# Kernel optimization log

Measured on AMD Instinct MI355X. Metric: run time of the kernel, lower is better.

## Reference

```python
import jax, jax.numpy as jnp
import numpy as np

N, NODE_DIM, EDGE_DIM, HID, NREL = 1024, 128, 32, 128, 16


def _sage(h, adj, W, b):
    # agg = mean over (weighted) neighbors: (adj @ h) / (deg + 1e-6)
    agg = (adj @ h) / (jnp.sum(adj, axis=1, keepdims=True) + 1e-6)
    return jax.nn.relu(jnp.concatenate([h, agg], axis=1) @ W.T + b)


def setup_inputs() -> dict:
    key = jax.random.key(0)
    ks = jax.random.split(key, 12)
    s1 = 1.0 / np.sqrt(2 * NODE_DIM)
    s2 = 1.0 / np.sqrt(2 * HID)
    s3 = 1.0 / np.sqrt(2 * HID + EDGE_DIM)
    s4 = 1.0 / np.sqrt(HID)
    return {
        "node_feat": jax.random.normal(ks[0], (N, NODE_DIM), jnp.float32),
        "edge_feat": jax.random.normal(ks[1], (N, N, EDGE_DIM), jnp.float32),
        "adj": jax.random.uniform(ks[2], (N, N), jnp.float32),
        "W_g1": jax.random.normal(ks[3], (HID, 2 * NODE_DIM), jnp.float32) * s1,
        "b_g1": jax.random.normal(ks[4], (HID,), jnp.float32) * s1,
        "W_g2": jax.random.normal(ks[5], (HID, 2 * HID), jnp.float32) * s2,
        "b_g2": jax.random.normal(ks[6], (HID,), jnp.float32) * s2,
        "W_c1": jax.random.normal(ks[7], (HID, 2 * HID + EDGE_DIM), jnp.float32) * s3,
        "b_c1": jax.random.normal(ks[8], (HID,), jnp.float32) * s3,
        "W_c2": jax.random.normal(ks[9], (NREL, HID), jnp.float32) * s4,
        "b_c2": jax.random.normal(ks[10], (NREL,), jnp.float32) * s4,
    }


def reference(node_feat, edge_feat, adj, W_g1, b_g1, W_g2, b_g2, W_c1, b_c1, W_c2, b_c2):
    h = _sage(node_feat, adj, W_g1, b_g1)          # [N, HID]
    h = _sage(h, adj, W_g2, b_g2)                  # [N, HID]
    H = h.shape[1]
    # Split first classifier layer over [h_i ; h_j ; e_ij] to avoid a huge concat.
    Wa, Wb, We = W_c1[:, :H], W_c1[:, H:2 * H], W_c1[:, 2 * H:]
    pre = ((h @ Wa.T)[:, None, :]
           + (h @ Wb.T)[None, :, :]
           + jnp.einsum('ije,he->ijh', edge_feat, We)
           + b_c1)                                  # [N, N, HID]
    logits = jax.nn.relu(pre) @ W_c2.T + b_c2       # [N, N, NREL]
    # diagonal (i == j) stays zero, matching the skipped loop iterations
    n = logits.shape[0]
    mask = 1.0 - jnp.eye(n, dtype=logits.dtype)
    return logits * mask[:, :, None]
```

## Files before the change

kernel.cpp:

```cpp
#include <hip/hip_runtime.h>
#include <hip/hip_bf16.h>
#include <stdint.h>

constexpr int NN = 1024;
constexpr int DD = 128;
constexpr int EDIM = 32;
constexpr int NR = 16;

using short4v = __attribute__((ext_vector_type(4))) short;
using short8v = __attribute__((ext_vector_type(8))) short;
using f32x4   = __attribute__((ext_vector_type(4))) float;

__device__ __forceinline__ short f2bf(float x) {
  __hip_bfloat16 h = __float2bfloat16(x);
  return __builtin_bit_cast(short, h);
}

__device__ __forceinline__ void gl_lds16(const void* g, void* l) {
  __builtin_amdgcn_global_load_lds(
      (const __attribute__((address_space(1))) unsigned int*)(uintptr_t)g,
      (__attribute__((address_space(3))) unsigned int*)(uint32_t)(uintptr_t)l,
      16, 0, 0);
}

__global__ __launch_bounds__(256) void k_rowsum(const float* __restrict__ adj,
                                                float* __restrict__ rsinv) {
  int i = blockIdx.x, t = threadIdx.x;
  const float4* row = (const float4*)(adj + (size_t)i * NN);
  float4 v = row[t];
  float s = v.x + v.y + v.z + v.w;
  #pragma unroll
  for (int off = 32; off > 0; off >>= 1) s += __shfl_down(s, off, 64);
  __shared__ float red[4];
  if ((t & 63) == 0) red[t >> 6] = s;
  __syncthreads();
  if (t == 0) rsinv[i] = 1.0f / (red[0] + red[1] + red[2] + red[3] + 1e-6f);
}

__global__ __launch_bounds__(256) void k_adjgemm(const float* __restrict__ adj,
                                                 const float* __restrict__ X,
                                                 float* __restrict__ part) {
  __shared__ float sadj[16][128];
  int t = threadIdx.x;
  int ic = blockIdx.x & 63, kc = blockIdx.x >> 6;
  int i0 = ic * 16, k0 = kc * 128;
  {
    int il = t >> 4;
    int kl = (t & 15) * 8;
    const float4* src = (const float4*)(adj + (size_t)(i0 + il) * NN + k0 + kl);
    *(float4*)&sadj[il][kl]     = src[0];
    *(float4*)&sadj[il][kl + 4] = src[1];
  }
  __syncthreads();
  int h = t & 127, ii = t >> 7;
  float acc[8] = {0,0,0,0,0,0,0,0};
  for (int k = 0; k < 128; k += 4) {
    float x0 = X[(size_t)(k0 + k) * DD + h];
    float x1 = X[(size_t)(k0 + k + 1) * DD + h];
    float x2 = X[(size_t)(k0 + k + 2) * DD + h];
    float x3 = X[(size_t)(k0 + k + 3) * DD + h];
    #pragma unroll
    for (int m = 0; m < 8; ++m) {
      int il = ii + m * 2;
      float4 a = *(const float4*)&sadj[il][k];
      acc[m] += a.x * x0 + a.y * x1 + a.z * x2 + a.w * x3;
    }
  }
  #pragma unroll
  for (int m = 0; m < 8; ++m)
    part[((size_t)kc * NN + (i0 + ii + m * 2)) * DD + h] = acc[m];
}

__global__ __launch_bounds__(256) void k_dense2f(const float* __restrict__ X,
                                                 const float* __restrict__ part,
                                                 const float* __restrict__ rsinv,
                                                 const float* __restrict__ W,
                                                 const float* __restrict__ b,
                                                 float* __restrict__ out) {
  __shared__ float sagg[2][128];
  int t = threadIdx.x;
  int ig = t >> 7, h = t & 127;
  int i = blockIdx.x * 2 + ig;
  {
    float s = 0.f;
    #pragma unroll
    for (int kc = 0; kc < 8; ++kc) s += part[(size_t)kc * NN * DD + (size_t)i * DD + h];
    sagg[ig][h] = s * rsinv[i];
  }
  __syncthreads();
  const float4* xr = (const float4*)(X + (size_t)i * DD);
  const float4* ar = (const float4*)(&sagg[ig][0]);
  const float4* w1 = (const float4*)(W + (size_t)h * 256);
  const float4* w2 = (const float4*)(W + (size_t)h * 256 + DD);
  float acc = b[h];
  #pragma unroll 8
  for (int k = 0; k < 32; ++k) {
    float4 x = xr[k], w = w1[k];
    acc += x.x * w.x + x.y * w.y + x.z * w.z + x.w * w.w;
  }
  #pragma unroll 8
  for (int k = 0; k < 32; ++k) {
    float4 y = ar[k], w = w2[k];
    acc += y.x * w.x + y.y * w.y + y.z * w.z + y.w * w.w;
  }
  out[(size_t)i * DD + h] = fmaxf(acc, 0.f);
}

__global__ __launch_bounds__(256) void k_ab(const float* __restrict__ h2,
                                            const float* __restrict__ Wc1,
                                            const float* __restrict__ bc1,
                                            float* __restrict__ Aib,
                                            float* __restrict__ Bmat) {
  int t = threadIdx.x;
  int i = blockIdx.x * 2 + (t >> 7), h = t & 127;
  const float4* xr = (const float4*)(h2 + (size_t)i * DD);
  const float4* wa = (const float4*)(Wc1 + (size_t)h * 288);
  const float4* wb = (const float4*)(Wc1 + (size_t)h * 288 + 128);
  float aa = bc1[h], bb = 0.f;
  #pragma unroll 8
  for (int k = 0; k < 32; ++k) {
    float4 x = xr[k];
    float4 a = wa[k], b2 = wb[k];
    aa += x.x * a.x + x.y * a.y + x.z * a.z + x.w * a.w;
    bb += x.x * b2.x + x.y * b2.y + x.z * b2.z + x.w * b2.w;
  }
  Aib[(size_t)i * DD + h] = aa;
  Bmat[(size_t)i * DD + h] = bb;
}


#define EDGE_BODY(T, OFF, VMN) do {                                           \
    float4 e0_, e1_;                                                          \
    asm volatile("s_waitcnt vmcnt(" #VMN ")\n\t"                              \
                 "ds_read_b128 %0, %2 offset:" #OFF "\n\t"                    \
                 "ds_read_b128 %1, %3 offset:" #OFF "\n\t"                    \
                 "s_waitcnt lgkmcnt(0)"                                       \
                 : "=&v"(e0_), "=&v"(e1_)                                     \
                 : "v"(ea0), "v"(ea1)                                         \
                 : "memory");                                                 \
    __builtin_amdgcn_sched_barrier(0);                                        \
    { int tpf_ = (T) + 3 > 15 ? 15 : (T) + 3;                                 \
      const char* src_ = ebl + (size_t)tpf_ * 131072;                         \
      gl_lds16(src_, esw + (OFF));                                            \
      gl_lds16(src_ + 1024, esw + (OFF) + 1024); }                            \
    __builtin_amdgcn_sched_barrier(0);                                        \
    short8v ef_;                                                              \
    ef_[0]=f2bf(e0_.x); ef_[1]=f2bf(e0_.y); ef_[2]=f2bf(e0_.z); ef_[3]=f2bf(e0_.w); \
    ef_[4]=f2bf(e1_.x); ef_[5]=f2bf(e1_.y); ef_[6]=f2bf(e1_.z); ef_[7]=f2bf(e1_.w); \
    int i_ = i0 + (T);                                                        \
    const float* ap_ = aibs + (T) * 128 + 4 * g;                              \
    _Pragma("unroll")                                                         \
    for (int n = 0; n < 8; ++n) {                                             \
      float4 av_ = *(const float4*)(ap_ + 16 * n);                            \
      f32x4 ci_;                                                              \
      ci_[0] = av_.x + bjv[n].x; ci_[1] = av_.y + bjv[n].y;                   \
      ci_[2] = av_.z + bjv[n].z; ci_[3] = av_.w + bjv[n].w;                   \
      f32x4 acc_ = __builtin_amdgcn_mfma_f32_16x16x32_bf16(weF[n], ef_, ci_, 0, 0, 0); \
      short4v pk_;                                                            \
      pk_[0] = f2bf(fmaxf(acc_[0], 0.f)); pk_[1] = f2bf(fmaxf(acc_[1], 0.f)); \
      pk_[2] = f2bf(fmaxf(acc_[2], 0.f)); pk_[3] = f2bf(fmaxf(acc_[3], 0.f)); \
      *(short4v*)(psm + (((n >> 1) << 10) + ((n & 1) << 9) + wroff)) = pk_;   \
    }                                                                         \
    f32x4 acc2_;                                                              \
    acc2_[0] = bc2v.x; acc2_[1] = bc2v.y; acc2_[2] = bc2v.z; acc2_[3] = bc2v.w; \
    _Pragma("unroll")                                                         \
    for (int kk = 0; kk < 4; ++kk) {                                          \
      short8v pb_ = *(short8v*)(psm + ((kk << 10) + rdP));                    \
      acc2_ = __builtin_amdgcn_mfma_f32_16x16x32_bf16(wcF[kk], pb_, acc2_, 0, 0, 0); \
    }                                                                         \
    bool diag_ = (j == i_);                                                   \
    float4 o_;                                                                \
    o_.x = diag_ ? 0.f : acc2_[0];                                            \
    o_.y = diag_ ? 0.f : acc2_[1];                                            \
    o_.z = diag_ ? 0.f : acc2_[2];                                            \
    o_.w = diag_ ? 0.f : acc2_[3];                                            \
    *(float4*)(out + ((size_t)i_ * NN + j) * NR + 4 * g) = o_;                \
  } while (0)

__global__ __launch_bounds__(256, 3) void k_edge(const float* __restrict__ edge,
                                                 const float* __restrict__ Wc1,
                                                 const float* __restrict__ Wc2,
                                                 const float* __restrict__ bc2,
                                                 const float* __restrict__ Aib,
                                                 const float* __restrict__ Bmat,
                                                 float* __restrict__ out) {
  __shared__ __align__(16) char esm[4][3][2048];
  __shared__ __align__(16) char psm_all[4][4096];
  __shared__ __align__(16) float aibs[16 * 128];
  int tid = threadIdx.x;
  int w = tid >> 6, lane = tid & 63;
  int c = lane & 15, g = lane >> 4;
  int ig = blockIdx.x >> 4, jg = blockIdx.x & 15;
  int i0 = ig * 16;
  int j0w = jg * 64 + w * 16;
  int j = j0w + c;

  {
    int ii = tid >> 4, h8 = (tid & 15) * 8;
    const float4* s = (const float4*)(Aib + (size_t)(i0 + ii) * DD + h8);
    *(float4*)(aibs + ii * 128 + h8)     = s[0];
    *(float4*)(aibs + ii * 128 + h8 + 4) = s[1];
  }
  __syncthreads();

  short8v weF[8];
  #pragma unroll
  for (int n = 0; n < 8; ++n) {
    const float* p = Wc1 + (size_t)(16 * n + c) * 288 + 256 + 8 * g;
    float4 f0 = *(const float4*)p;
    float4 f1 = *(const float4*)(p + 4);
    short8v s;
    s[0]=f2bf(f0.x); s[1]=f2bf(f0.y); s[2]=f2bf(f0.z); s[3]=f2bf(f0.w);
    s[4]=f2bf(f1.x); s[5]=f2bf(f1.y); s[6]=f2bf(f1.z); s[7]=f2bf(f1.w);
    weF[n] = s;
  }
  short8v wcF[4];
  #pragma unroll
  for (int kk = 0; kk < 4; ++kk) {
    const float* p = Wc2 + (size_t)c * DD + 32 * kk + 8 * g;
    float4 f0 = *(const float4*)p;
    float4 f1 = *(const float4*)(p + 4);
    short8v s;
    s[0]=f2bf(f0.x); s[1]=f2bf(f0.y); s[2]=f2bf(f0.z); s[3]=f2bf(f0.w);
    s[4]=f2bf(f1.x); s[5]=f2bf(f1.y); s[6]=f2bf(f1.z); s[7]=f2bf(f1.w);
    wcF[kk] = s;
  }
  float4 bc2v = *(const float4*)(bc2 + 4 * g);
  float4 bjv[8];
  #pragma unroll
  for (int n = 0; n < 8; ++n)
    bjv[n] = *(const float4*)(Bmat + (size_t)j * DD + 16 * n + 4 * g);

  char* esw = &esm[w][0][0];
  char* psm = &psm_all[w][0];
  const char* ebl = (const char*)edge + ((size_t)i0 * NN + j0w) * (EDIM * 4)
                    + ((lane * 16) ^ (((lane >> 3) & 7) << 4));
  int rd0 = c * 128 + ((g * 32)      ^ ((c & 7) << 4));
  int rd1 = c * 128 + ((g * 32 + 16) ^ ((c & 7) << 4));
  int ldsb = (int)(uint32_t)(uintptr_t)esw;
  int ea0 = ldsb + rd0;
  int ea1 = ldsb + rd1;
  int wroff = (c << 4) + ((g & 1) << 3) + ((g >> 1) << 8);
  int rdP   = (g << 8) + (c << 4);

  gl_lds16(ebl,                  esw);
  gl_lds16(ebl + 1024,           esw + 1024);
  gl_lds16(ebl + 131072,         esw + 2048);
  gl_lds16(ebl + 131072 + 1024,  esw + 3072);
  gl_lds16(ebl + 262144,         esw + 4096);
  gl_lds16(ebl + 262144 + 1024,  esw + 5120);

  EDGE_BODY(0, 0, 4);
  EDGE_BODY(1, 2048, 5);
  EDGE_BODY(2, 4096, 6);
  #pragma unroll 1
  for (int t = 3; t < 15; t += 3) {
    EDGE_BODY(t,     0, 6);
    EDGE_BODY(t + 1, 2048, 6);
    EDGE_BODY(t + 2, 4096, 6);
  }
  EDGE_BODY(15, 0, 6);
}

extern "C" void kernel_launch(void* const* d_in, const int* in_sizes, int n_in,
                              void* d_out, int out_size, void* d_ws, size_t ws_size,
                              hipStream_t stream) {
  const float* node_feat = (const float*)d_in[0];
  const float* edge_feat = (const float*)d_in[1];
  const float* adj  = (const float*)d_in[2];
  const float* W_g1 = (const float*)d_in[3];
  const float* b_g1 = (const float*)d_in[4];
  const float* W_g2 = (const float*)d_in[5];
  const float* b_g2 = (const float*)d_in[6];
  const float* W_c1 = (const float*)d_in[7];
  const float* b_c1 = (const float*)d_in[8];
  const float* W_c2 = (const float*)d_in[9];
  const float* b_c2 = (const float*)d_in[10];
  float* out = (float*)d_out;

  float* ws    = (float*)d_ws;
  float* rsinv = ws;
  float* part  = ws + 1024;
  float* h1    = part + 8 * NN * DD;
  float* h2    = h1 + NN * DD;
  float* Aib   = h2 + NN * DD;
  float* Bmat  = Aib + NN * DD;

  k_rowsum<<<NN, 256, 0, stream>>>(adj, rsinv);
  k_adjgemm<<<512, 256, 0, stream>>>(adj, node_feat, part);
  k_dense2f<<<512, 256, 0, stream>>>(node_feat, part, rsinv, W_g1, b_g1, h1);
  k_adjgemm<<<512, 256, 0, stream>>>(adj, h1, part);
  k_dense2f<<<512, 256, 0, stream>>>(h1, part, rsinv, W_g2, b_g2, h2);
  k_ab<<<512, 256, 0, stream>>>(h2, W_c1, b_c1, Aib, Bmat);
  k_edge<<<1024, 256, 0, stream>>>(edge_feat, W_c1, W_c2, b_c2, Aib, Bmat, out);
}
```

Baseline: 139.9 us.

## Deepen edge prefetch pipeline, software-pipeline second MFMA, fuse small prologue kernels

```diff
diff --git a/kernel.cpp b/kernel.cpp
--- a/kernel.cpp
+++ b/kernel.cpp
@@ -21,20 +21,6 @@
       (const __attribute__((address_space(1))) unsigned int*)(uintptr_t)g,
       (__attribute__((address_space(3))) unsigned int*)(uint32_t)(uintptr_t)l,
       16, 0, 0);
-}
-
-__global__ __launch_bounds__(256) void k_rowsum(const float* __restrict__ adj,
-                                                float* __restrict__ rsinv) {
-  int i = blockIdx.x, t = threadIdx.x;
-  const float4* row = (const float4*)(adj + (size_t)i * NN);
-  float4 v = row[t];
-  float s = v.x + v.y + v.z + v.w;
-  #pragma unroll
-  for (int off = 32; off > 0; off >>= 1) s += __shfl_down(s, off, 64);
-  __shared__ float red[4];
-  if ((t & 63) == 0) red[t >> 6] = s;
-  __syncthreads();
-  if (t == 0) rsinv[i] = 1.0f / (red[0] + red[1] + red[2] + red[3] + 1e-6f);
 }
 
 __global__ __launch_bounds__(256) void k_adjgemm(const float* __restrict__ adj,
@@ -71,21 +57,34 @@
     part[((size_t)kc * NN + (i0 + ii + m * 2)) * DD + h] = acc[m];
 }
 
-__global__ __launch_bounds__(256) void k_dense2f(const float* __restrict__ X,
-                                                 const float* __restrict__ part,
-                                                 const float* __restrict__ rsinv,
-                                                 const float* __restrict__ W,
-                                                 const float* __restrict__ b,
-                                                 float* __restrict__ out) {
+__global__ __launch_bounds__(256) void k_dense1(const float* __restrict__ X,
+                                                const float* __restrict__ part,
+                                                const float* __restrict__ adj,
+                                                const float* __restrict__ W,
+                                                const float* __restrict__ b,
+                                                float* __restrict__ out,
+                                                float* __restrict__ rsinv) {
   __shared__ float sagg[2][128];
+  __shared__ float red[4];
   int t = threadIdx.x;
   int ig = t >> 7, h = t & 127;
   int i = blockIdx.x * 2 + ig;
   {
-    float s = 0.f;
+    const float4* ar = (const float4*)(adj + (size_t)i * NN);
+    float4 v0 = ar[h * 2], v1 = ar[h * 2 + 1];
+    float s = v0.x + v0.y + v0.z + v0.w + v1.x + v1.y + v1.z + v1.w;
     #pragma unroll
-    for (int kc = 0; kc < 8; ++kc) s += part[(size_t)kc * NN * DD + (size_t)i * DD + h];
-    sagg[ig][h] = s * rsinv[i];
+    for (int off = 32; off > 0; off >>= 1) s += __shfl_down(s, off, 64);
+    if ((t & 63) == 0) red[t >> 6] = s;
+  }
+  __syncthreads();
+  float rs = 1.0f / (red[ig * 2] + red[ig * 2 + 1] + 1e-6f);
+  if (h == 0) rsinv[i] = rs;
+  {
+    float ss = 0.f;
+    #pragma unroll
+    for (int kc = 0; kc < 8; ++kc) ss += part[(size_t)kc * NN * DD + (size_t)i * DD + h];
+    sagg[ig][h] = ss * rs;
   }
   __syncthreads();
   const float4* xr = (const float4*)(X + (size_t)i * DD);
@@ -106,14 +105,47 @@
   out[(size_t)i * DD + h] = fmaxf(acc, 0.f);
 }
 
-__global__ __launch_bounds__(256) void k_ab(const float* __restrict__ h2,
-                                            const float* __restrict__ Wc1,
-                                            const float* __restrict__ bc1,
-                                            float* __restrict__ Aib,
-                                            float* __restrict__ Bmat) {
+__global__ __launch_bounds__(256) void k_dense2ab(const float* __restrict__ X,
+                                                  const float* __restrict__ part,
+                                                  const float* __restrict__ rsinv,
+                                                  const float* __restrict__ W,
+                                                  const float* __restrict__ b,
+                                                  const float* __restrict__ Wc1,
+                                                  const float* __restrict__ bc1,
+                                                  float* __restrict__ Aib,
+                                                  float* __restrict__ Bmat) {
+  __shared__ float sagg[2][128];
+  __shared__ float sh2[2][128];
   int t = threadIdx.x;
-  int i = blockIdx.x * 2 + (t >> 7), h = t & 127;
-  const float4* xr = (const float4*)(h2 + (size_t)i * DD);
+  int ig = t >> 7, h = t & 127;
+  int i = blockIdx.x * 2 + ig;
+  {
+    float ss = 0.f;
+    #pragma unroll
+    for (int kc = 0; kc < 8; ++kc) ss += part[(size_t)kc * NN * DD + (size_t)i * DD + h];
+    sagg[ig][h] = ss * rsinv[i];
+  }
+  __syncthreads();
+  {
+    const float4* xr = (const float4*)(X + (size_t)i * DD);
+    const float4* ar = (const float4*)(&sagg[ig][0]);
+    const float4* w1 = (const float4*)(W + (size_t)h * 256);
+    const float4* w2 = (const float4*)(W + (size_t)h * 256 + DD);
+    float acc = b[h];
+    #pragma unroll 8
+    for (int k = 0; k < 32; ++k) {
+      float4 x = xr[k], w = w1[k];
+      acc += x.x * w.x + x.y * w.y + x.z * w.z + x.w * w.w;
+    }
+    #pragma unroll 8
+    for (int k = 0; k < 32; ++k) {
+      float4 y = ar[k], w = w2[k];
+      acc += y.x * w.x + y.y * w.y + y.z * w.z + y.w * w.w;
+    }
+    sh2[ig][h] = fmaxf(acc, 0.f);
+  }
+  __syncthreads();
+  const float4* xr = (const float4*)(&sh2[ig][0]);
   const float4* wa = (const float4*)(Wc1 + (size_t)h * 288);
   const float4* wb = (const float4*)(Wc1 + (size_t)h * 288 + 128);
   float aa = bc1[h], bb = 0.f;
@@ -129,7 +161,7 @@
 }
 
 
-#define EDGE_BODY(T, OFF, VMN) do {                                           \
+#define EDGE_BODY(T, OFF, VMN, PF) do {                                       \
     float4 e0_, e1_;                                                          \
     asm volatile("s_waitcnt vmcnt(" #VMN ")\n\t"                              \
                  "ds_read_b128 %0, %2 offset:" #OFF "\n\t"                    \
@@ -139,15 +171,16 @@
                  : "v"(ea0), "v"(ea1)                                         \
                  : "memory");                                                 \
     __builtin_amdgcn_sched_barrier(0);                                        \
-    { int tpf_ = (T) + 3 > 15 ? 15 : (T) + 3;                                 \
-      const char* src_ = ebl + (size_t)tpf_ * 131072;                         \
+    if (PF) {                                                                 \
+      const char* src_ = ebl + (size_t)((T) + 5) * 131072;                    \
       gl_lds16(src_, esw + (OFF));                                            \
-      gl_lds16(src_ + 1024, esw + (OFF) + 1024); }                            \
+      gl_lds16(src_ + 1024, esw + (OFF) + 1024);                              \
+    }                                                                         \
     __builtin_amdgcn_sched_barrier(0);                                        \
     short8v ef_;                                                              \
     ef_[0]=f2bf(e0_.x); ef_[1]=f2bf(e0_.y); ef_[2]=f2bf(e0_.z); ef_[3]=f2bf(e0_.w); \
     ef_[4]=f2bf(e1_.x); ef_[5]=f2bf(e1_.y); ef_[6]=f2bf(e1_.z); ef_[7]=f2bf(e1_.w); \
-    int i_ = i0 + (T);                                                        \
+    char* pw_ = psm + (((T) & 1) << 12);                                      \
     const float* ap_ = aibs + (T) * 128 + 4 * g;                              \
     _Pragma("unroll")                                                         \
     for (int n = 0; n < 8; ++n) {                                             \
@@ -159,33 +192,42 @@
       short4v pk_;                                                            \
       pk_[0] = f2bf(fmaxf(acc_[0], 0.f)); pk_[1] = f2bf(fmaxf(acc_[1], 0.f)); \
       pk_[2] = f2bf(fmaxf(acc_[2], 0.f)); pk_[3] = f2bf(fmaxf(acc_[3], 0.f)); \
-      *(short4v*)(psm + (((n >> 1) << 10) + ((n & 1) << 9) + wroff)) = pk_;   \
+      *(short4v*)(pw_ + (((n >> 1) << 10) + ((n & 1) << 9) + wroff)) = pk_;   \
     }                                                                         \
-    f32x4 acc2_;                                                              \
-    acc2_[0] = bc2v.x; acc2_[1] = bc2v.y; acc2_[2] = bc2v.z; acc2_[3] = bc2v.w; \
+  } while (0)
+
+#define G2(G2T, OREG) do {                                                    \
+    f32x4 a2_;                                                                \
+    a2_[0] = bc2v.x; a2_[1] = bc2v.y; a2_[2] = bc2v.z; a2_[3] = bc2v.w;       \
+    const char* pp_ = psm + (((G2T) & 1) << 12);                              \
     _Pragma("unroll")                                                         \
     for (int kk = 0; kk < 4; ++kk) {                                          \
-      short8v pb_ = *(short8v*)(psm + ((kk << 10) + rdP));                    \
-      acc2_ = __builtin_amdgcn_mfma_f32_16x16x32_bf16(wcF[kk], pb_, acc2_, 0, 0, 0); \
+      short8v pb_ = *(const short8v*)(pp_ + ((kk << 10) + rdP));              \
+      a2_ = __builtin_amdgcn_mfma_f32_16x16x32_bf16(wcF[kk], pb_, a2_, 0, 0, 0); \
     }                                                                         \
-    bool diag_ = (j == i_);                                                   \
-    float4 o_;                                                                \
-    o_.x = diag_ ? 0.f : acc2_[0];                                            \
-    o_.y = diag_ ? 0.f : acc2_[1];                                            \
-    o_.z = diag_ ? 0.f : acc2_[2];                                            \
-    o_.w = diag_ ? 0.f : acc2_[3];                                            \
-    *(float4*)(out + ((size_t)i_ * NN + j) * NR + 4 * g) = o_;                \
+    bool dg_ = (j == i0 + (G2T));                                             \
+    OREG.x = dg_ ? 0.f : a2_[0];                                              \
+    OREG.y = dg_ ? 0.f : a2_[1];                                              \
+    OREG.z = dg_ ? 0.f : a2_[2];                                              \
+    OREG.w = dg_ ? 0.f : a2_[3];                                              \
   } while (0)
 
-__global__ __launch_bounds__(256, 3) void k_edge(const float* __restrict__ edge,
+#define FLUSH(BASE) do {                                                      \
+    *(float4*)(out + ((size_t)(i0 + (BASE) + 0) * NN + j) * NR + 4 * g) = o0; \
+    *(float4*)(out + ((size_t)(i0 + (BASE) + 1) * NN + j) * NR + 4 * g) = o1; \
+    *(float4*)(out + ((size_t)(i0 + (BASE) + 2) * NN + j) * NR + 4 * g) = o2; \
+    *(float4*)(out + ((size_t)(i0 + (BASE) + 3) * NN + j) * NR + 4 * g) = o3; \
+  } while (0)
+
+__global__ __launch_bounds__(256, 2) void k_edge(const float* __restrict__ edge,
                                                  const float* __restrict__ Wc1,
                                                  const float* __restrict__ Wc2,
                                                  const float* __restrict__ bc2,
                                                  const float* __restrict__ Aib,
                                                  const float* __restrict__ Bmat,
                                                  float* __restrict__ out) {
-  __shared__ __align__(16) char esm[4][3][2048];
-  __shared__ __align__(16) char psm_all[4][4096];
+  __shared__ __align__(16) char esm[4][5][2048];
+  __shared__ __align__(16) char psm_all[4][2][4096];
   __shared__ __align__(16) float aibs[16 * 128];
   int tid = threadIdx.x;
   int w = tid >> 6, lane = tid & 63;
@@ -201,7 +243,6 @@
     *(float4*)(aibs + ii * 128 + h8)     = s[0];
     *(float4*)(aibs + ii * 128 + h8 + 4) = s[1];
   }
-  __syncthreads();
 
   short8v weF[8];
   #pragma unroll
@@ -231,8 +272,10 @@
   for (int n = 0; n < 8; ++n)
     bjv[n] = *(const float4*)(Bmat + (size_t)j * DD + 16 * n + 4 * g);
 
+  __syncthreads();
+
   char* esw = &esm[w][0][0];
-  char* psm = &psm_all[w][0];
+  char* psm = &psm_all[w][0][0];
   const char* ebl = (const char*)edge + ((size_t)i0 * NN + j0w) * (EDIM * 4)
                     + ((lane * 16) ^ (((lane >> 3) & 7) << 4));
   int rd0 = c * 128 + ((g * 32)      ^ ((c & 7) << 4));
@@ -243,23 +286,36 @@
   int wroff = (c << 4) + ((g & 1) << 3) + ((g >> 1) << 8);
   int rdP   = (g << 8) + (c << 4);
 
-  gl_lds16(ebl,                  esw);
-  gl_lds16(ebl + 1024,           esw + 1024);
-  gl_lds16(ebl + 131072,         esw + 2048);
-  gl_lds16(ebl + 131072 + 1024,  esw + 3072);
-  gl_lds16(ebl + 262144,         esw + 4096);
-  gl_lds16(ebl + 262144 + 1024,  esw + 5120);
-
-  EDGE_BODY(0, 0, 4);
-  EDGE_BODY(1, 2048, 5);
-  EDGE_BODY(2, 4096, 6);
-  #pragma unroll 1
-  for (int t = 3; t < 15; t += 3) {
-    EDGE_BODY(t,     0, 6);
-    EDGE_BODY(t + 1, 2048, 6);
-    EDGE_BODY(t + 2, 4096, 6);
-  }
-  EDGE_BODY(15, 0, 6);
+  float4 o0, o1, o2, o3;
+
+  gl_lds16(ebl,                      esw);
+  gl_lds16(ebl + 1024,               esw + 1024);
+  gl_lds16(ebl + 1 * 131072,         esw + 2048);
+  gl_lds16(ebl + 1 * 131072 + 1024,  esw + 3072);
+  gl_lds16(ebl + 2 * 131072,         esw + 4096);
+  gl_lds16(ebl + 2 * 131072 + 1024,  esw + 5120);
+  gl_lds16(ebl + 3 * 131072,         esw + 6144);
+  gl_lds16(ebl + 3 * 131072 + 1024,  esw + 7168);
+  gl_lds16(ebl + 4 * 131072,         esw + 8192);
+  gl_lds16(ebl + 4 * 131072 + 1024,  esw + 9216);
+
+  EDGE_BODY(0,  0,    8, 1);
+  EDGE_BODY(1,  2048, 8, 1);  G2(0, o0);
+  EDGE_BODY(2,  4096, 8, 1);  G2(1, o1);
+  EDGE_BODY(3,  6144, 8, 1);  G2(2, o2);
+  EDGE_BODY(4,  8192, 8, 1);  G2(3, o3);  FLUSH(0);
+  EDGE_BODY(5,  0,    12, 1); G2(4, o0);
+  EDGE_BODY(6,  2048, 12, 1); G2(5, o1);
+  EDGE_BODY(7,  4096, 12, 1); G2(6, o2);
+  EDGE_BODY(8,  6144, 12, 1); G2(7, o3);  FLUSH(4);
+  EDGE_BODY(9,  8192, 12, 1); G2(8, o0);
+  EDGE_BODY(10, 0,    12, 1); G2(9, o1);
+  EDGE_BODY(11, 2048, 12, 0); G2(10, o2);
+  EDGE_BODY(12, 4096, 10, 0); G2(11, o3); FLUSH(8);
+  EDGE_BODY(13, 6144, 12, 0); G2(12, o0);
+  EDGE_BODY(14, 8192, 6, 0);  G2(13, o1);
+  EDGE_BODY(15, 0,    4, 0);  G2(14, o2);
+  G2(15, o3); FLUSH(12);
 }
 
 extern "C" void kernel_launch(void* const* d_in, const int* in_sizes, int n_in,
@@ -282,15 +338,12 @@
   float* rsinv = ws;
   float* part  = ws + 1024;
   float* h1    = part + 8 * NN * DD;
-  float* h2    = h1 + NN * DD;
-  float* Aib   = h2 + NN * DD;
+  float* Aib   = h1 + NN * DD;
   float* Bmat  = Aib + NN * DD;
 
-  k_rowsum<<<NN, 256, 0, stream>>>(adj, rsinv);
   k_adjgemm<<<512, 256, 0, stream>>>(adj, node_feat, part);
-  k_dense2f<<<512, 256, 0, stream>>>(node_feat, part, rsinv, W_g1, b_g1, h1);
+  k_dense1<<<512, 256, 0, stream>>>(node_feat, part, adj, W_g1, b_g1, h1, rsinv);
   k_adjgemm<<<512, 256, 0, stream>>>(adj, h1, part);
-  k_dense2f<<<512, 256, 0, stream>>>(h1, part, rsinv, W_g2, b_g2, h2);
-  k_ab<<<512, 256, 0, stream>>>(h2, W_c1, b_c1, Aib, Bmat);
+  k_dense2ab<<<512, 256, 0, stream>>>(h1, part, rsinv, W_g2, b_g2, W_c1, b_c1, Aib, Bmat);
   k_edge<<<1024, 256, 0, stream>>>(edge_feat, W_c1, W_c2, b_c2, Aib, Bmat, out);
 }
```

New measurement: 129.5 us. 1.08x faster.
